# Kernel tuning notes

Hardware: AMD Instinct MI355X
Metric: run time of the kernel (lower is better)

The kernel has to match this reference:

```python
import jax, jax.numpy as jnp
import numpy as np

# LeNet-5 custom connectivity between S2 (6 ch) and C3 (16 ch): MAP[i, o] = 1 if input ch i feeds output ch o
MAP_INFO = np.array([
    [1, 0, 0, 0, 1, 1, 1, 0, 0, 1, 1, 1, 1, 0, 1, 1],
    [1, 1, 0, 0, 0, 1, 1, 1, 0, 0, 1, 1, 1, 1, 0, 1],
    [1, 1, 1, 0, 0, 0, 1, 1, 1, 0, 0, 1, 0, 1, 1, 1],
    [0, 1, 1, 1, 0, 0, 1, 1, 1, 1, 0, 0, 1, 0, 1, 1],
    [0, 0, 1, 1, 1, 0, 0, 1, 1, 1, 1, 0, 1, 1, 0, 1],
    [0, 0, 0, 1, 1, 1, 0, 0, 1, 1, 1, 1, 0, 1, 1, 1],
], dtype=np.float32)  # [6, 16]

SCALE = 1.7159
SLOPE = 2.0 / 3.0


def _conv(x, w):
    # x: [B, Cin, H, W], w: [Cout, Cin, kh, kw], VALID padding, stride 1
    return jax.lax.conv_general_dilated(
        x, w, window_strides=(1, 1), padding='VALID',
        dimension_numbers=('NCHW', 'OIHW', 'NCHW'))


def _subsample(x, w, b):
    # 2x2 average pool then per-channel affine (trainable scale/bias)
    B, C, H, W = x.shape
    p = x.reshape(B, C, H // 2, 2, W // 2, 2).mean(axis=(3, 5))
    return p * w[None, :, None, None] + b[None, :, None, None]


def _act(x):
    return SCALE * jnp.tanh(SLOPE * x)


def setup_inputs() -> dict:
    key = jax.random.key(0)
    ks = jax.random.split(key, 16)
    B = 8192

    def unif(k, shape, fan_in):
        return (jax.random.uniform(k, shape, dtype=jnp.float32) * 4.8 - 2.4) / fan_in

    x = jax.random.normal(ks[0], (B, 1, 32, 32), dtype=jnp.float32)
    c1_w = unif(ks[1], (6, 1, 5, 5), 25 * 1)
    c1_b = jax.random.uniform(ks[2], (6,), dtype=jnp.float32) * 0.1
    s2_w = unif(ks[3], (6,), 4)
    s2_b = jax.random.uniform(ks[4], (6,), dtype=jnp.float32)
    c3_w = unif(ks[5], (16, 6, 5, 5), 25 * 6)
    c3_b = jax.random.uniform(ks[6], (16,), dtype=jnp.float32) * 0.1
    s4_w = unif(ks[7], (16,), 4)
    s4_b = jax.random.uniform(ks[8], (16,), dtype=jnp.float32)
    c5_w = unif(ks[9], (120, 16, 5, 5), 25 * 16)
    c5_b = jax.random.uniform(ks[10], (120,), dtype=jnp.float32) * 0.1
    f6_w = unif(ks[11], (84, 120), 120)
    f6_b = jax.random.uniform(ks[12], (84,), dtype=jnp.float32) * 0.1
    rbf_w = jax.random.uniform(ks[13], (84, 10), dtype=jnp.float32)
    return dict(x=x, c1_w=c1_w, c1_b=c1_b, s2_w=s2_w, s2_b=s2_b,
                c3_w=c3_w, c3_b=c3_b, s4_w=s4_w, s4_b=s4_b,
                c5_w=c5_w, c5_b=c5_b, f6_w=f6_w, f6_b=f6_b, rbf_w=rbf_w)


def reference(x, c1_w, c1_b, s2_w, s2_b, c3_w, c3_b, s4_w, s4_b,
              c5_w, c5_b, f6_w, f6_b, rbf_w):
    # C1: 1->6 conv5, replicate padding 2 -> [B,6,32,32]
    xp = jnp.pad(x, ((0, 0), (0, 0), (2, 2), (2, 2)), mode='edge')
    h = _conv(xp, c1_w) + c1_b[None, :, None, None]
    # S2 + squashing act -> [B,6,16,16]
    h = _act(_subsample(h, s2_w, s2_b))
    # C3: sparse-connectivity conv expressed as dense conv with masked weights -> [B,16,12,12]
    mask = jnp.asarray(MAP_INFO.T)[:, :, None, None]  # [16,6,1,1]
    h = _conv(h, c3_w * mask) + c3_b[None, :, None, None]
    # S4 + act -> [B,16,6,6]
    h = _act(_subsample(h, s4_w, s4_b))
    # C5: 16->120 conv5 -> [B,120,1,1]
    h = _conv(h, c5_w) + c5_b[None, :, None, None]
    h = h.reshape(-1, 120)
    # F6 + act -> [B,84]
    h = _act(h @ f6_w.T + f6_b)
    # RBF output: squared euclidean distance to class prototypes -> [B,10]
    out = jnp.sum((h[:, :, None] - rbf_w[None, :, :]) ** 2, axis=1)
    return out
```

## Files before the change

### kernel.cpp

```cpp
#include <hip/hip_runtime.h>
#include <math.h>

typedef _Float16 h16;
typedef h16  h8v __attribute__((ext_vector_type(8)));
typedef h16  h4v __attribute__((ext_vector_type(4)));
typedef h16  h2v __attribute__((ext_vector_type(2)));
typedef float f4v __attribute__((ext_vector_type(4)));
typedef unsigned int u32;

#if defined(__has_builtin)
#if __has_builtin(__builtin_amdgcn_fdot2)
#define FDOT2(a,b,c) __builtin_amdgcn_fdot2((a),(b),(c),false)
#endif
#endif
#ifndef FDOT2
#define FDOT2(a,b,c) ((c) + (float)(a).x*(float)(b).x + (float)(a).y*(float)(b).y)
#endif

#define WS_K1H  0
#define WS_B1   216
#define WS_B3   224
#define WS_W3H  240
#define WS_W5H  2544
#define WS_F6H  35312
#define WS_RBFT 41456

#define L_B3    0
#define L_C5B   64
#define L_F6B   576
#define L_S2H   960
#define L_A5    960
#define L_HB    960
#define L_XPADH 14784
#define L_S4    20160
#define L_A6    20160
#define LDS_TOTAL 26304

__device__ const unsigned char MASK16[16] = {7,14,28,56,49,35,15,30,60,57,51,39,27,54,45,63};

__device__ __forceinline__ float squash(float x) {
    float E = __expf(1.33333333f * x);
    return 1.7159f - 3.4318f * __builtin_amdgcn_rcpf(1.0f + E);
}

__global__ __launch_bounds__(256) void prep_kernel(
    const float* __restrict__ c1_w, const float* __restrict__ c1_b,
    const float* __restrict__ s2_w, const float* __restrict__ s2_b,
    const float* __restrict__ c3_w, const float* __restrict__ c3_b,
    const float* __restrict__ s4_w, const float* __restrict__ s4_b,
    const float* __restrict__ c5_w, const float* __restrict__ f6_w,
    const float* __restrict__ rbf_w,
    float* __restrict__ ws)
{
    const int gid = blockIdx.x * 256 + threadIdx.x;
    const int gstr = gridDim.x * 256;
    h16* K1H = (h16*)ws;
    for (int idx = gid; idx < 216; idx += gstr) {
        int c = idx / 36, r = idx - c * 36;
        int u = r / 6, v = r - u * 6;
        float s = 0.f;
        #pragma unroll
        for (int dy = 0; dy < 2; ++dy)
            #pragma unroll
            for (int dx = 0; dx < 2; ++dx) {
                int ky = u - dy, kx = v - dx;
                if (ky >= 0 && ky < 5 && kx >= 0 && kx < 5)
                    s += c1_w[(c * 5 + ky) * 5 + kx];
            }
        K1H[idx] = (h16)(0.25f * s * s2_w[c]);
    }
    if (gid < 6)  ws[WS_B1 + gid] = s2_w[gid] * c1_b[gid] + s2_b[gid];
    if (gid < 16) ws[WS_B3 + gid] = s4_w[gid] * c3_b[gid] + s4_b[gid];
    h16* W3H = (h16*)(ws + WS_W3H);
    for (int idx = gid; idx < 4608; idx += gstr) {
        int i = idx / 768, r = idx - i * 768;
        int n = r / 48, k = r - n * 48;
        float val = 0.f;
        if (k < 36) {
            int u = k / 6, v = k - u * 6;
            float s = 0.f;
            #pragma unroll
            for (int dy = 0; dy < 2; ++dy)
                #pragma unroll
                for (int dx = 0; dx < 2; ++dx) {
                    int ky = u - dy, kx = v - dx;
                    if (ky >= 0 && ky < 5 && kx >= 0 && kx < 5)
                        s += c3_w[((n * 6 + i) * 5 + ky) * 5 + kx];
                }
            val = ((MASK16[n] >> i) & 1) ? 0.25f * s4_w[n] * s : 0.f;
        }
        W3H[idx] = (h16)val;
    }
    h16* W5H = (h16*)(ws + WS_W5H);
    for (int idx = gid; idx < 65536; idx += gstr) {
        int i = idx >> 12, r = idx & 4095;
        int n = r >> 5, k = r & 31;
        float val = (n < 120 && k < 25) ? c5_w[n * 400 + i * 25 + k] : 0.f;
        W5H[idx] = (h16)val;
    }
    h16* F6H = (h16*)(ws + WS_F6H);
    for (int idx = gid; idx < 12288; idx += gstr) {
        int n = idx >> 7, k = idx & 127;
        float val = (n < 84 && k < 120) ? f6_w[n * 120 + k] : 0.f;
        F6H[idx] = (h16)val;
    }
    for (int idx = gid; idx < 840; idx += gstr) {
        int k = idx / 10, c = idx - k * 10;
        ws[WS_RBFT + c * 84 + k] = rbf_w[idx];
    }
}

__global__ __launch_bounds__(256, 6) void lenet_kernel(
    const float* __restrict__ x,
    const float* __restrict__ c5_b, const float* __restrict__ f6_b,
    const float* __restrict__ ws,
    float* __restrict__ out)
{
    __shared__ __align__(16) char smem[LDS_TOTAL];
    float* s_b3  = (float*)(smem + L_B3);
    float* s_c5b = (float*)(smem + L_C5B);
    float* s_f6b = (float*)(smem + L_F6B);
    h16*  XPADH  = (h16*)(smem + L_XPADH);
    h16*  S2H    = (h16*)(smem + L_S2H);
    h16*  S4     = (h16*)(smem + L_S4);
    h16*  A5     = (h16*)(smem + L_A5);
    h16*  A6     = (h16*)(smem + L_A6);
    float* HB    = (float*)(smem + L_HB);

    const int tid  = threadIdx.x;
    const int wave = __builtin_amdgcn_readfirstlane(tid >> 6);
    const int lane = tid & 63;
    const int quad = lane >> 4;
    const int lr   = lane & 15;

    if (tid < 16)  s_b3[tid] = ws[WS_B3 + tid];
    if (tid < 128) s_c5b[tid] = (tid < 120) ? c5_b[tid] : 0.f;
    if (tid < 96)  s_f6b[tid] = (tid < 84) ? f6_b[tid] : 0.f;
    const float* xb = x + (size_t)blockIdx.x * 4096;
    for (int idx = tid; idx < 2880; idx += 256) {
        int img = idx / 720, r2 = idx - img * 720;
        int u = r2 / 20, v2 = r2 - u * 20;
        int sy = min(max(u - 2, 0), 31);
        int c0 = min(max(2 * v2 - 2, 0), 31);
        int c1 = min(max(2 * v2 - 1, 0), 31);
        const float* xr = xb + img * 1024 + sy * 32;
        h2v hv; hv.x = (h16)xr[c0]; hv.y = (h16)xr[c1];
        *(h2v*)(XPADH + img * 1440 + u * 40 + 2 * v2) = hv;
    }
    __syncthreads();

    {
        int py = tid >> 4, px = tid & 15;
        const h2v* K1H = (const h2v*)ws;
        #pragma unroll 1
        for (int img = 0; img < 4; ++img) {
            const h16* basep = XPADH + img * 1440 + (2 * py) * 40 + 2 * px;
            h2v win2[18];
            #pragma unroll
            for (int u = 0; u < 6; ++u)
                #pragma unroll
                for (int p = 0; p < 3; ++p)
                    win2[u * 3 + p] = *(const h2v*)(basep + u * 40 + 2 * p);
            #pragma unroll
            for (int c = 0; c < 6; ++c) {
                float acc = ws[WS_B1 + c];
                #pragma unroll
                for (int j = 0; j < 18; ++j)
                    acc = FDOT2(win2[j], K1H[c * 18 + j], acc);
                S2H[img * 1728 + c * 288 + py * 18 + px] = (h16)squash(acc);
            }
        }
    }
    __syncthreads();

    {
        const h16* W3H = (const h16*)(ws + WS_W3H);
        int o0, o1, o2, o3;
        {
            int k0 = 8 * quad;
            int u0 = k0 / 6, v0 = k0 - u0 * 6;  o0 = u0 * 18 + v0;
            int k1 = k0 + 2;
            int u1 = k1 / 6, v1 = k1 - u1 * 6;  o1 = u1 * 18 + v1;
            int k2 = k0 + 4;
            int u2 = k2 / 6, v2 = k2 - u2 * 6;  o2 = u2 * 18 + v2;
            int k3 = k0 + 6;
            int u3 = k3 / 6, v3 = k3 - u3 * 6;  o3 = u3 * 18 + v3;
        }
        int baseh0, baseh1, baseh2;
        {
            int m0 = wave * 16 + lr;
            int i0 = m0 / 36, p0 = m0 - i0 * 36;
            baseh0 = i0 * 1728 + (2 * (p0 / 6)) * 18 + 2 * (p0 % 6);
            int m1 = (wave + 4) * 16 + lr;
            int i1 = m1 / 36, p1 = m1 - i1 * 36;
            baseh1 = i1 * 1728 + (2 * (p1 / 6)) * 18 + 2 * (p1 % 6);
            int m2 = 128 + lr;
            int i2 = m2 / 36, p2 = m2 - i2 * 36;
            baseh2 = i2 * 1728 + (2 * (p2 / 6)) * 18 + 2 * (p2 % 6);
        }
        f4v cacc0 = {}, cacc1 = {}, cacc2 = {};
        const bool w0 = (wave == 0);
        #pragma unroll
        for (int i = 0; i < 6; ++i) {
            const h16* bbase = W3H + i * 768 + lr * 48;
            h8v w3a = *(const h8v*)(bbase + quad * 8);
            h4v w3b = *(const h4v*)(bbase + 32 + quad * 4);
            const h16* bp0 = S2H + baseh0 + i * 288;
            {
                union { u32 u[4]; h8v h; } av;
                av.u[0] = *(const u32*)(bp0 + o0);
                av.u[1] = *(const u32*)(bp0 + o1);
                av.u[2] = *(const u32*)(bp0 + o2);
                av.u[3] = *(const u32*)(bp0 + o3);
                cacc0 = __builtin_amdgcn_mfma_f32_16x16x32_f16(av.h, w3a, cacc0, 0, 0, 0);
                union { u32 u[2]; h4v h; } av2;
                av2.u[0] = *(const u32*)(bp0 + 92);
                av2.u[1] = *(const u32*)(bp0 + 94);
                cacc0 = __builtin_amdgcn_mfma_f32_16x16x16f16(av2.h, w3b, cacc0, 0, 0, 0);
            }
            const h16* bp1 = S2H + baseh1 + i * 288;
            {
                union { u32 u[4]; h8v h; } av;
                av.u[0] = *(const u32*)(bp1 + o0);
                av.u[1] = *(const u32*)(bp1 + o1);
                av.u[2] = *(const u32*)(bp1 + o2);
                av.u[3] = *(const u32*)(bp1 + o3);
                cacc1 = __builtin_amdgcn_mfma_f32_16x16x32_f16(av.h, w3a, cacc1, 0, 0, 0);
                union { u32 u[2]; h4v h; } av2;
                av2.u[0] = *(const u32*)(bp1 + 92);
                av2.u[1] = *(const u32*)(bp1 + 94);
                cacc1 = __builtin_amdgcn_mfma_f32_16x16x16f16(av2.h, w3b, cacc1, 0, 0, 0);
            }
            if (w0) {
                const h16* bp2 = S2H + baseh2 + i * 288;
                union { u32 u[4]; h8v h; } av;
                av.u[0] = *(const u32*)(bp2 + o0);
                av.u[1] = *(const u32*)(bp2 + o1);
                av.u[2] = *(const u32*)(bp2 + o2);
                av.u[3] = *(const u32*)(bp2 + o3);
                cacc2 = __builtin_amdgcn_mfma_f32_16x16x32_f16(av.h, w3a, cacc2, 0, 0, 0);
                union { u32 u[2]; h4v h; } av2;
                av2.u[0] = *(const u32*)(bp2 + 92);
                av2.u[1] = *(const u32*)(bp2 + 94);
                cacc2 = __builtin_amdgcn_mfma_f32_16x16x16f16(av2.h, w3b, cacc2, 0, 0, 0);
            }
        }
        float b3v = s_b3[lr];
        {
            #pragma unroll
            for (int r = 0; r < 4; ++r) {
                int m = wave * 16 + quad * 4 + r;
                int img = m / 36, pos = m - img * 36;
                S4[img * 672 + lr * 42 + pos] = (h16)squash(cacc0[r] + b3v);
            }
            #pragma unroll
            for (int r = 0; r < 4; ++r) {
                int m = (wave + 4) * 16 + quad * 4 + r;
                int img = m / 36, pos = m - img * 36;
                S4[img * 672 + lr * 42 + pos] = (h16)squash(cacc1[r] + b3v);
            }
            if (w0) {
                #pragma unroll
                for (int r = 0; r < 4; ++r) {
                    int m = 128 + quad * 4 + r;
                    int img = m / 36, pos = m - img * 36;
                    S4[img * 672 + lr * 42 + pos] = (h16)squash(cacc2[r] + b3v);
                }
            }
        }
    }
    __syncthreads();

    {
        {
            int m = tid >> 4, i = tid & 15;
            int img = m >> 2, q = m & 3, qy = q >> 1, qx = q & 1;
            const h16* s4b = S4 + img * 672 + i * 42 + qy * 6 + qx;
            h16* dst = A5 + m * 520 + i * 32;
            #pragma unroll
            for (int c = 0; c < 4; ++c) {
                h8v v;
                #pragma unroll
                for (int j = 0; j < 8; ++j) {
                    int k = c * 8 + j;
                    v[j] = (k < 25) ? s4b[(k / 5) * 6 + (k % 5)] : (h16)0.f;
                }
                *(h8v*)(dst + c * 8) = v;
            }
        }
        __syncthreads();
        const h16* W5H = (const h16*)(ws + WS_W5H);
        f4v dacc0 = {}, dacc1 = {};
        #pragma unroll
        for (int i = 0; i < 16; ++i) {
            h8v bf0 = *(const h8v*)(W5H + i * 4096 + (wave * 32 + lr) * 32 + quad * 8);
            h8v bf1 = *(const h8v*)(W5H + i * 4096 + (wave * 32 + 16 + lr) * 32 + quad * 8);
            h8v af0 = *(const h8v*)(A5 + lr * 520 + i * 32 + quad * 8);
            dacc0 = __builtin_amdgcn_mfma_f32_16x16x32_f16(af0, bf0, dacc0, 0, 0, 0);
            dacc1 = __builtin_amdgcn_mfma_f32_16x16x32_f16(af0, bf1, dacc1, 0, 0, 0);
        }
        if (tid < 64) {
            int m = tid >> 2, j = tid & 3;
            *(u32*)(A6 + m * 136 + 120 + 2 * j) = 0u;
        }
        {
            int n0 = wave * 32 + lr;
            if (n0 < 120) {
                int tt = n0 / 30, cb = (n0 - tt * 30) * 4;
                float bias = s_c5b[n0];
                #pragma unroll
                for (int r = 0; r < 4; ++r) {
                    int m = quad * 4 + r;
                    A6[((m >> 2) * 4 + tt) * 136 + cb + (m & 3)] = (h16)(dacc0[r] + bias);
                }
            }
            int n1 = wave * 32 + 16 + lr;
            if (n1 < 120) {
                int tt = n1 / 30, cb = (n1 - tt * 30) * 4;
                float bias = s_c5b[n1];
                #pragma unroll
                for (int r = 0; r < 4; ++r) {
                    int m = quad * 4 + r;
                    A6[((m >> 2) * 4 + tt) * 136 + cb + (m & 3)] = (h16)(dacc1[r] + bias);
                }
            }
        }
    }
    __syncthreads();

    {
        const h16* F6H = (const h16*)(ws + WS_F6H);
        f4v eacc0 = {}, eacc1 = {};
        const bool w2 = (wave < 2);
        #pragma unroll
        for (int kc = 0; kc < 4; ++kc) {
            h8v a8 = *(const h8v*)(A6 + lr * 136 + kc * 32 + quad * 8);
            h8v b0 = *(const h8v*)(F6H + (wave * 16 + lr) * 128 + kc * 32 + quad * 8);
            eacc0 = __builtin_amdgcn_mfma_f32_16x16x32_f16(a8, b0, eacc0, 0, 0, 0);
            if (w2) {
                h8v b1 = *(const h8v*)(F6H + ((wave + 4) * 16 + lr) * 128 + kc * 32 + quad * 8);
                eacc1 = __builtin_amdgcn_mfma_f32_16x16x32_f16(a8, b1, eacc1, 0, 0, 0);
            }
        }
        {
            int n = wave * 16 + lr;
            float bias = s_f6b[n];
            #pragma unroll
            for (int r = 0; r < 4; ++r) {
                int m = quad * 4 + r;
                HB[m * 88 + n] = squash(eacc0[r] + bias);
            }
        }
        if (w2) {
            int n = (wave + 4) * 16 + lr;
            if (n < 84) {
                float bias = s_f6b[n];
                #pragma unroll
                for (int r = 0; r < 4; ++r) {
                    int m = quad * 4 + r;
                    HB[m * 88 + n] = squash(eacc1[r] + bias);
                }
            }
        }
    }
    __syncthreads();

    if (tid < 160) {
        int m = tid / 10, cls = tid - m * 10;
        const float4* hr = (const float4*)(HB + m * 88);
        const float4* pr = (const float4*)(ws + WS_RBFT + cls * 84);
        float a = 0.f;
        #pragma unroll
        for (int u = 0; u < 21; ++u) {
            float4 hv = hr[u], pv = pr[u];
            float dx = hv.x - pv.x, dy = hv.y - pv.y;
            float dz = hv.z - pv.z, dw = hv.w - pv.w;
            a += dx * dx + dy * dy + dz * dz + dw * dw;
        }
        out[(size_t)blockIdx.x * 160 + tid] = a;
    }
}

extern "C" void kernel_launch(void* const* d_in, const int* in_sizes, int n_in,
                              void* d_out, int out_size, void* d_ws, size_t ws_size,
                              hipStream_t stream) {
    (void)n_in; (void)out_size; (void)ws_size;
    const float* x     = (const float*)d_in[0];
    const float* c1_w  = (const float*)d_in[1];
    const float* c1_b  = (const float*)d_in[2];
    const float* s2_w  = (const float*)d_in[3];
    const float* s2_b  = (const float*)d_in[4];
    const float* c3_w  = (const float*)d_in[5];
    const float* c3_b  = (const float*)d_in[6];
    const float* s4_w  = (const float*)d_in[7];
    const float* s4_b  = (const float*)d_in[8];
    const float* c5_w  = (const float*)d_in[9];
    const float* c5_b  = (const float*)d_in[10];
    const float* f6_w  = (const float*)d_in[11];
    const float* f6_b  = (const float*)d_in[12];
    const float* rbf_w = (const float*)d_in[13];
    float* out = (float*)d_out;
    float* ws  = (float*)d_ws;

    const int B = in_sizes[0] / 1024;

    prep_kernel<<<256, 256, 0, stream>>>(c1_w, c1_b, s2_w, s2_b, c3_w, c3_b,
                                         s4_w, s4_b, c5_w, f6_w, rbf_w, ws);
    lenet_kernel<<<B / 4, 256, 0, stream>>>(x, c5_b, f6_b, ws, out);
}
```

Before: 144.1 us.

## Shrink LDS footprint, pack C5 K dimension densely, raise occupancy to 8 blocks

The padded input buffer now holds two images at a time instead of four. The second pair is held in registers and written after the first pair's C1 pass, and the buffer aliases the S4/A6 region. The C5 im2col is packed contiguously at 25 taps per channel, so the MFMA loop runs 13 K-blocks instead of 16, and the prep kernel repacks the weights to match. Cutting LDS from about 26KB to 20KB allows launch bounds to request 8 blocks per CU. The cost is an extra barrier and C1 phase, plus scalar 2-byte LDS stores in the A5 build, which may cause bank conflicts.

```diff
diff --git a/kernel.cpp b/kernel.cpp
--- a/kernel.cpp
+++ b/kernel.cpp
@@ -22,19 +22,19 @@
 #define WS_B3   224
 #define WS_W3H  240
 #define WS_W5H  2544
-#define WS_F6H  35312
-#define WS_RBFT 41456
+#define WS_F6H  29168
+#define WS_RBFT 35312
 
 #define L_B3    0
 #define L_C5B   64
-#define L_F6B   576
-#define L_S2H   960
-#define L_A5    960
-#define L_HB    960
-#define L_XPADH 14784
-#define L_S4    20160
-#define L_A6    20160
-#define LDS_TOTAL 26304
+#define L_F6B   544
+#define L_S2H   880
+#define L_A5    880
+#define L_HB    880
+#define L_XPAD  14704
+#define L_S4    14704
+#define L_A6    14704
+#define LDS_TOTAL 20080
 
 __device__ const unsigned char MASK16[16] = {7,14,28,56,49,35,15,30,60,57,51,39,27,54,45,63};
 
@@ -92,10 +92,11 @@
         W3H[idx] = (h16)val;
     }
     h16* W5H = (h16*)(ws + WS_W5H);
-    for (int idx = gid; idx < 65536; idx += gstr) {
-        int i = idx >> 12, r = idx & 4095;
+    for (int idx = gid; idx < 53248; idx += gstr) {
+        int kb = idx >> 12, r = idx & 4095;
         int n = r >> 5, k = r & 31;
-        float val = (n < 120 && k < 25) ? c5_w[n * 400 + i * 25 + k] : 0.f;
+        int kg = kb * 32 + k;
+        float val = (n < 120 && kg < 400) ? c5_w[n * 400 + kg] : 0.f;
         W5H[idx] = (h16)val;
     }
     h16* F6H = (h16*)(ws + WS_F6H);
@@ -110,7 +111,7 @@
     }
 }
 
-__global__ __launch_bounds__(256, 6) void lenet_kernel(
+__global__ __launch_bounds__(256, 8) void lenet_kernel(
     const float* __restrict__ x,
     const float* __restrict__ c5_b, const float* __restrict__ f6_b,
     const float* __restrict__ ws,
@@ -120,7 +121,7 @@
     float* s_b3  = (float*)(smem + L_B3);
     float* s_c5b = (float*)(smem + L_C5B);
     float* s_f6b = (float*)(smem + L_F6B);
-    h16*  XPADH  = (h16*)(smem + L_XPADH);
+    h16*  XPAD   = (h16*)(smem + L_XPAD);
     h16*  S2H    = (h16*)(smem + L_S2H);
     h16*  S4     = (h16*)(smem + L_S4);
     h16*  A5     = (h16*)(smem + L_A5);
@@ -134,40 +135,83 @@
     const int lr   = lane & 15;
 
     if (tid < 16)  s_b3[tid] = ws[WS_B3 + tid];
-    if (tid < 128) s_c5b[tid] = (tid < 120) ? c5_b[tid] : 0.f;
-    if (tid < 96)  s_f6b[tid] = (tid < 84) ? f6_b[tid] : 0.f;
+    if (tid < 120) s_c5b[tid] = c5_b[tid];
+    if (tid < 84)  s_f6b[tid] = f6_b[tid];
     const float* xb = x + (size_t)blockIdx.x * 4096;
-    for (int idx = tid; idx < 2880; idx += 256) {
-        int img = idx / 720, r2 = idx - img * 720;
-        int u = r2 / 20, v2 = r2 - u * 20;
-        int sy = min(max(u - 2, 0), 31);
-        int c0 = min(max(2 * v2 - 2, 0), 31);
-        int c1 = min(max(2 * v2 - 1, 0), 31);
-        const float* xr = xb + img * 1024 + sy * 32;
-        h2v hv; hv.x = (h16)xr[c0]; hv.y = (h16)xr[c1];
-        *(h2v*)(XPADH + img * 1440 + u * 40 + 2 * v2) = hv;
+    h2v r1[6];
+    #pragma unroll
+    for (int it = 0; it < 6; ++it) {
+        int idx = tid + it * 256;
+        if (idx < 1296) {
+            int img2 = idx / 648, r2 = idx - img2 * 648;
+            int u = r2 / 18, v = r2 - u * 18;
+            int sy = min(max(u - 2, 0), 31);
+            int c0 = min(max(2 * v - 2, 0), 31);
+            int c1 = min(max(2 * v - 1, 0), 31);
+            const float* xr0 = xb + img2 * 1024 + sy * 32;
+            h2v hv0; hv0.x = (h16)xr0[c0]; hv0.y = (h16)xr0[c1];
+            *(h2v*)(XPAD + img2 * 1296 + u * 36 + 2 * v) = hv0;
+            const float* xr1 = xr0 + 2048;
+            h2v hv1; hv1.x = (h16)xr1[c0]; hv1.y = (h16)xr1[c1];
+            r1[it] = hv1;
+        }
     }
     __syncthreads();
 
     {
-        int py = tid >> 4, px = tid & 15;
+        int py = tid & 15, px = tid >> 4;
         const h2v* K1H = (const h2v*)ws;
         #pragma unroll 1
-        for (int img = 0; img < 4; ++img) {
-            const h16* basep = XPADH + img * 1440 + (2 * py) * 40 + 2 * px;
+        for (int img2 = 0; img2 < 2; ++img2) {
+            const h16* basep = XPAD + img2 * 1296 + (2 * py) * 36 + 2 * px;
             h2v win2[18];
             #pragma unroll
             for (int u = 0; u < 6; ++u)
                 #pragma unroll
                 for (int p = 0; p < 3; ++p)
-                    win2[u * 3 + p] = *(const h2v*)(basep + u * 40 + 2 * p);
+                    win2[u * 3 + p] = *(const h2v*)(basep + u * 36 + 2 * p);
             #pragma unroll
             for (int c = 0; c < 6; ++c) {
                 float acc = ws[WS_B1 + c];
                 #pragma unroll
                 for (int j = 0; j < 18; ++j)
                     acc = FDOT2(win2[j], K1H[c * 18 + j], acc);
-                S2H[img * 1728 + c * 288 + py * 18 + px] = (h16)squash(acc);
+                S2H[img2 * 1728 + c * 288 + py * 18 + px] = (h16)squash(acc);
+            }
+        }
+    }
+    __syncthreads();
+
+    #pragma unroll
+    for (int it = 0; it < 6; ++it) {
+        int idx = tid + it * 256;
+        if (idx < 1296) {
+            int img2 = idx / 648, r2 = idx - img2 * 648;
+            int u = r2 / 18, v = r2 - u * 18;
+            *(h2v*)(XPAD + img2 * 1296 + u * 36 + 2 * v) = r1[it];
+        }
+    }
+    __syncthreads();
+
+    {
+        int py = tid & 15, px = tid >> 4;
+        const h2v* K1H = (const h2v*)ws;
+        #pragma unroll 1
+        for (int img2 = 0; img2 < 2; ++img2) {
+            const h16* basep = XPAD + img2 * 1296 + (2 * py) * 36 + 2 * px;
+            h2v win2[18];
+            #pragma unroll
+            for (int u = 0; u < 6; ++u)
+                #pragma unroll
+                for (int p = 0; p < 3; ++p)
+                    win2[u * 3 + p] = *(const h2v*)(basep + u * 36 + 2 * p);
+            #pragma unroll
+            for (int c = 0; c < 6; ++c) {
+                float acc = ws[WS_B1 + c];
+                #pragma unroll
+                for (int j = 0; j < 18; ++j)
+                    acc = FDOT2(win2[j], K1H[c * 18 + j], acc);
+                S2H[(2 + img2) * 1728 + c * 288 + py * 18 + px] = (h16)squash(acc);
             }
         }
     }
@@ -276,26 +320,24 @@
             int m = tid >> 4, i = tid & 15;
             int img = m >> 2, q = m & 3, qy = q >> 1, qx = q & 1;
             const h16* s4b = S4 + img * 672 + i * 42 + qy * 6 + qx;
-            h16* dst = A5 + m * 520 + i * 32;
-            #pragma unroll
-            for (int c = 0; c < 4; ++c) {
-                h8v v;
-                #pragma unroll
-                for (int j = 0; j < 8; ++j) {
-                    int k = c * 8 + j;
-                    v[j] = (k < 25) ? s4b[(k / 5) * 6 + (k % 5)] : (h16)0.f;
-                }
-                *(h8v*)(dst + c * 8) = v;
+            h16* dst = A5 + m * 424 + i * 25;
+            #pragma unroll
+            for (int k = 0; k < 25; ++k)
+                dst[k] = s4b[(k / 5) * 6 + (k % 5)];
+            if (i == 15) {
+                #pragma unroll
+                for (int j = 0; j < 12; ++j)
+                    *(u32*)(A5 + m * 424 + 400 + 2 * j) = 0u;
             }
         }
         __syncthreads();
         const h16* W5H = (const h16*)(ws + WS_W5H);
         f4v dacc0 = {}, dacc1 = {};
         #pragma unroll
-        for (int i = 0; i < 16; ++i) {
+        for (int i = 0; i < 13; ++i) {
             h8v bf0 = *(const h8v*)(W5H + i * 4096 + (wave * 32 + lr) * 32 + quad * 8);
             h8v bf1 = *(const h8v*)(W5H + i * 4096 + (wave * 32 + 16 + lr) * 32 + quad * 8);
-            h8v af0 = *(const h8v*)(A5 + lr * 520 + i * 32 + quad * 8);
+            h8v af0 = *(const h8v*)(A5 + lr * 424 + i * 32 + quad * 8);
             dacc0 = __builtin_amdgcn_mfma_f32_16x16x32_f16(af0, bf0, dacc0, 0, 0, 0);
             dacc1 = __builtin_amdgcn_mfma_f32_16x16x32_f16(af0, bf1, dacc1, 0, 0, 0);
         }
```

After: 138.2 us. 1.04x faster.
